# Kernel optimization log

Hardware: AMD Instinct MI355X
Metric: run time of the kernel (lower is better)

The kernel has to match this reference:

```python
import jax, jax.numpy as jnp
import numpy as np

TOP_K = 32
SCALE_FACTOR = 8.0
NEG_INF = -1e18


def setup_inputs() -> dict:
    key = jax.random.key(0)
    kq, kk, kv = jax.random.split(key, 3)
    B, H, S, D = 2, 16, 2048, 64
    q = jax.random.normal(kq, (B, H, S, D), dtype=jnp.float32)
    k = jax.random.normal(kk, (B, H, S, D), dtype=jnp.float32)
    v = jax.random.normal(kv, (B, H, S, D), dtype=jnp.float32)
    return {"q": q, "k": k, "v": v}


def reference(q, k, v):
    # scores: [B, H, Sq, Sk]
    scores = jnp.einsum("bhqd,bhkd->bhqk", q, k) / SCALE_FACTOR
    # torch code clamps top_k against key.size()[-1] == head dim D (quirk);
    # with TOP_K=32 < D=64 the clamp is inactive.
    top_k = min(TOP_K, k.shape[-1])
    topv, _ = jax.lax.top_k(scores, top_k)            # [B,H,Sq,top_k], sorted desc
    thresh = topv[..., -1:]                            # k-th largest per query row
    mask_k = scores < thresh                           # True -> masked out
    scores = jnp.where(mask_k, NEG_INF, scores)
    attn = jax.nn.softmax(scores, axis=-1)
    context = jnp.einsum("bhqk,bhkd->bhqd", attn, v)
    return context, attn, mask_k
```

## Files before the change

### kernel.cpp

```cpp
#include <hip/hip_runtime.h>
#include <math.h>

namespace {
constexpr int kS = 2048;
constexpr int kD = 64;
constexpr int kBH = 32;
constexpr int kTopK = 32;
constexpr int kPadBins = 2112;
constexpr int kCandCap = 128;
constexpr int kKeepCap = 64;
constexpr size_t kCtxElems  = (size_t)kBH * kS * kD;
constexpr size_t kAttnElems = (size_t)kBH * kS * kS;
}

typedef float f2 __attribute__((ext_vector_type(2)));

__device__ __forceinline__ unsigned sortable_bits(float x) {
  unsigned u = __float_as_uint(x);
  return u ^ ((u & 0x80000000u) ? 0xFFFFFFFFu : 0x80000000u);
}

__global__ __launch_bounds__(256) void qk_scores(const float* __restrict__ q,
                                                 const float* __restrict__ k,
                                                 float* __restrict__ scores) {
  __shared__ float QsT[32][260];
  __shared__ float KsT[32][132];
  const int bh  = blockIdx.z;
  const int q0  = blockIdx.y * 256;
  const int k0  = blockIdx.x * 128;
  const int tid = threadIdx.x;
  const float* qg = q + ((size_t)bh * kS + q0) * kD;
  const float* kg = k + ((size_t)bh * kS + k0) * kD;

  const int ty16 = (tid >> 4) * 16;
  const int tx8  = (tid & 15) * 8;
  f2 acc[16][4] = {};

  for (int half = 0; half < 2; ++half) {
    if (half) __syncthreads();
#pragma unroll
    for (int rnd = 0; rnd < 8; ++rnd) {
      int flat = rnd * 1024 + tid * 4;
      int r = flat >> 5;
      int c = flat & 31;
      float4 qv = *(const float4*)(qg + r * kD + half * 32 + c);
      QsT[c + 0][r] = qv.x;
      QsT[c + 1][r] = qv.y;
      QsT[c + 2][r] = qv.z;
      QsT[c + 3][r] = qv.w;
    }
#pragma unroll
    for (int rnd = 0; rnd < 4; ++rnd) {
      int flat = rnd * 1024 + tid * 4;
      int r = flat >> 5;
      int c = flat & 31;
      float4 kv = *(const float4*)(kg + r * kD + half * 32 + c);
      KsT[c + 0][r] = kv.x;
      KsT[c + 1][r] = kv.y;
      KsT[c + 2][r] = kv.z;
      KsT[c + 3][r] = kv.w;
    }
    __syncthreads();

#pragma unroll
    for (int kk = 0; kk < 32; ++kk) {
      float a[16];
      f2 b[4];
      *(float4*)(&a[0])  = *(const float4*)(&QsT[kk][ty16]);
      *(float4*)(&a[4])  = *(const float4*)(&QsT[kk][ty16 + 4]);
      *(float4*)(&a[8])  = *(const float4*)(&QsT[kk][ty16 + 8]);
      *(float4*)(&a[12]) = *(const float4*)(&QsT[kk][ty16 + 12]);
      float4 b0 = *(const float4*)(&KsT[kk][tx8]);
      float4 b1 = *(const float4*)(&KsT[kk][tx8 + 4]);
      b[0] = f2{b0.x, b0.y};
      b[1] = f2{b0.z, b0.w};
      b[2] = f2{b1.x, b1.y};
      b[3] = f2{b1.z, b1.w};
#pragma unroll
      for (int i = 0; i < 16; ++i) {
        const f2 as = {a[i], a[i]};
#pragma unroll
        for (int j2 = 0; j2 < 4; ++j2)
          acc[i][j2] += as * b[j2];
      }
    }
  }

#pragma unroll
  for (int i = 0; i < 16; ++i) {
    float* orow = scores + ((size_t)bh * kS + q0 + ty16 + i) * kS + k0 + tx8;
    float4 o0 = make_float4(acc[i][0].x * 0.125f, acc[i][0].y * 0.125f,
                            acc[i][1].x * 0.125f, acc[i][1].y * 0.125f);
    float4 o1 = make_float4(acc[i][2].x * 0.125f, acc[i][2].y * 0.125f,
                            acc[i][3].x * 0.125f, acc[i][3].y * 0.125f);
    *(float4*)(orow)     = o0;
    *(float4*)(orow + 4) = o1;
  }
}

__global__ __launch_bounds__(256) void topk_softmax(const float* __restrict__ v,
                                                    float* __restrict__ ctx,
                                                    float* __restrict__ attn,
                                                    float* __restrict__ mask) {
  __shared__ unsigned s_hist[4][kPadBins];
  __shared__ float    s_cand[4][kCandCap];
  __shared__ int      s_kidx[4][kKeepCap];
  __shared__ float    s_kw[4][kKeepCap];
  __shared__ unsigned s_nc[4];

  const int tid  = threadIdx.x;
  const int wid  = tid >> 6;
  const int lane = tid & 63;
  const int row  = blockIdx.x * 4 + wid;
  const int bh   = row >> 11;
  unsigned* hist = s_hist[wid];

  const float* srow = attn + (size_t)row * kS;
  float locv[32];
#pragma unroll
  for (int g = 0; g < 8; ++g)
    *(float4*)(&locv[g * 4]) = *(const float4*)(srow + g * 256 + lane * 4);

#pragma unroll
  for (int j = 0; j < 33; ++j) hist[j * 64 + lane] = 0u;
  if (lane == 0) s_nc[wid] = 0u;

  float pmax = locv[0];
#pragma unroll
  for (int j = 0; j < 32; ++j) {
    unsigned b = sortable_bits(locv[j]) >> 21;
    atomicAdd(&hist[b + (b >> 5)], 1u);
    pmax = fmaxf(pmax, locv[j]);
  }
#pragma unroll
  for (int off = 32; off >= 1; off >>= 1)
    pmax = fmaxf(pmax, __shfl_xor(pmax, off));

  asm volatile("s_waitcnt lgkmcnt(0)" ::: "memory");

  unsigned lsum = 0;
#pragma unroll
  for (int j = 0; j < 32; ++j) lsum += hist[lane * 33 + j];
  unsigned sfx = lsum;
#pragma unroll
  for (int off = 1; off < 64; off <<= 1) {
    unsigned z = __shfl_down(sfx, off);
    if (lane + off < 64) sfx += z;
  }
  const unsigned above = sfx - lsum;

  int bstar = 0, gabove = 0;
  const bool ispiv = (sfx >= (unsigned)kTopK) && (above < (unsigned)kTopK);
  if (ispiv) {
    unsigned run = above;
    for (int j = 31; j >= 0; --j) {
      unsigned h = hist[lane * 33 + j];
      if (run < (unsigned)kTopK && run + h >= (unsigned)kTopK) {
        bstar  = lane * 32 + j;
        gabove = (int)run;
      }
      run += h;
    }
  }
  const unsigned long long pm = __ballot(ispiv);
  const int psrc = __ffsll(pm) - 1;
  bstar  = __shfl(bstar, psrc);
  gabove = __shfl(gabove, psrc);

#pragma unroll
  for (int j = 0; j < 32; ++j) {
    unsigned b = sortable_bits(locv[j]) >> 21;
    if ((int)b == bstar) {
      unsigned p = atomicAdd(&s_nc[wid], 1u);
      if (p < (unsigned)kCandCap) s_cand[wid][p] = locv[j];
    }
  }
  asm volatile("s_waitcnt lgkmcnt(0)" ::: "memory");
  const int m = (int)min(s_nc[wid], (unsigned)kCandCap);

  const float x0 = (lane < m) ? s_cand[wid][lane] : 0.0f;
  const float x1 = (lane + 64 < m) ? s_cand[wid][lane + 64] : 0.0f;
  int g0 = 0, e0 = 0, g1 = 0, e1 = 0;
  for (int j = 0; j < m; ++j) {
    float y = s_cand[wid][j];
    g0 += (y > x0); e0 += (y == x0);
    g1 += (y > x1); e1 += (y == x1);
  }
  const bool win0 = (lane < m) &&
                    (gabove + g0 < kTopK) && (gabove + g0 + e0 >= kTopK);
  const bool win1 = (lane + 64 < m) &&
                    (gabove + g1 < kTopK) && (gabove + g1 + e1 >= kTopK);
  const unsigned long long wm0 = __ballot(win0);
  const unsigned long long wm1 = __ballot(win1);
  float t32;
  if (wm0 != 0ull)      t32 = __shfl(x0, __ffsll(wm0) - 1);
  else if (wm1 != 0ull) t32 = __shfl(x1, __ffsll(wm1) - 1);
  else                  t32 = pmax;

  const unsigned long long below = (1ull << lane) - 1ull;
  float w32[32];
  float psum = 0.0f;
  int nkbase = 0;
#pragma unroll
  for (int j = 0; j < 32; ++j) {
    const bool keep = (locv[j] >= t32);
    const float wv = keep ? __expf(locv[j] - pmax) : 0.0f;
    w32[j] = wv;
    psum += wv;
    const unsigned long long mk = __ballot(keep);
    if (keep) {
      const int slot = nkbase + (int)__popcll(mk & below);
      if (slot < kKeepCap) {
        s_kidx[wid][slot] = (j >> 2) * 256 + lane * 4 + (j & 3);
        s_kw[wid][slot]   = wv;
      }
    }
    nkbase += (int)__popcll(mk);
  }
  const int nk = nkbase < kKeepCap ? nkbase : kKeepCap;
#pragma unroll
  for (int off = 32; off >= 1; off >>= 1)
    psum += __shfl_xor(psum, off);
  const float invZ = 1.0f / psum;

  float* arow = attn + (size_t)row * kS;
  float* mrow = mask + (size_t)row * kS;
#pragma unroll
  for (int g = 0; g < 8; ++g) {
    float4 a = make_float4(w32[g*4+0] * invZ, w32[g*4+1] * invZ,
                           w32[g*4+2] * invZ, w32[g*4+3] * invZ);
    float4 mm = make_float4(locv[g*4+0] >= t32 ? 0.f : 1.f,
                            locv[g*4+1] >= t32 ? 0.f : 1.f,
                            locv[g*4+2] >= t32 ? 0.f : 1.f,
                            locv[g*4+3] >= t32 ? 0.f : 1.f);
    *(float4*)(arow + g * 256 + lane * 4) = a;
    *(float4*)(mrow + g * 256 + lane * 4) = mm;
  }

  asm volatile("s_waitcnt lgkmcnt(0)" ::: "memory");
  const float* vb = v + ((size_t)bh * kS) * kD + lane;
  float acc = 0.0f;
  int c = 0;
  for (; c + 8 <= nk; c += 8) {
    float w[8], vv[8];
    int   ii[8];
#pragma unroll
    for (int u = 0; u < 8; ++u) {
      w[u]  = s_kw[wid][c + u];
      ii[u] = s_kidx[wid][c + u];
    }
#pragma unroll
    for (int u = 0; u < 8; ++u)
      vv[u] = vb[(size_t)ii[u] * kD];
#pragma unroll
    for (int u = 0; u < 8; ++u)
      acc += w[u] * vv[u];
  }
  for (; c < nk; ++c)
    acc += s_kw[wid][c] * vb[(size_t)s_kidx[wid][c] * kD];
  ctx[(size_t)row * kD + lane] = acc * invZ;
}

extern "C" void kernel_launch(void* const* d_in, const int* in_sizes, int n_in,
                              void* d_out, int out_size, void* d_ws, size_t ws_size,
                              hipStream_t stream) {
  const float* q = (const float*)d_in[0];
  const float* k = (const float*)d_in[1];
  const float* v = (const float*)d_in[2];
  float* out  = (float*)d_out;
  float* ctx  = out;
  float* attn = out + kCtxElems;
  float* mask = attn + kAttnElems;

  dim3 g1(kS / 128, kS / 256, kBH);
  qk_scores<<<g1, 256, 0, stream>>>(q, k, attn);
  topk_softmax<<<dim3(kBH * kS / 4), 256, 0, stream>>>(v, ctx, attn, mask);
}
```

Measured before the change: 1.409 ms.

## Pre-transpose Q into scratch and stream it from global in QK kernel

```diff
diff --git a/kernel.cpp b/kernel.cpp
--- a/kernel.cpp
+++ b/kernel.cpp
@@ -20,81 +20,89 @@
   return u ^ ((u & 0x80000000u) ? 0xFFFFFFFFu : 0x80000000u);
 }
 
-__global__ __launch_bounds__(256) void qk_scores(const float* __restrict__ q,
-                                                 const float* __restrict__ k,
-                                                 float* __restrict__ scores) {
-  __shared__ float QsT[32][260];
-  __shared__ float KsT[32][132];
+__global__ __launch_bounds__(256) void qt_transpose(const float* __restrict__ q,
+                                                    float* __restrict__ qt) {
+  __shared__ float T[kD][130];
+  const int bh  = blockIdx.z;
+  const int r0  = blockIdx.x * 128;
+  const int tid = threadIdx.x;
+  const float* qg = q + ((size_t)bh * kS + r0) * kD;
+#pragma unroll
+  for (int rnd = 0; rnd < 8; ++rnd) {
+    int flat = rnd * 1024 + tid * 4;
+    int r = flat >> 6, c = flat & 63;
+    float4 v = *(const float4*)(qg + flat);
+    T[c + 0][r] = v.x; T[c + 1][r] = v.y;
+    T[c + 2][r] = v.z; T[c + 3][r] = v.w;
+  }
+  __syncthreads();
+  const int wid = tid >> 6, lane = tid & 63;
+#pragma unroll
+  for (int p = 0; p < 8; ++p) {
+    int d = p * 8 + wid * 2 + (lane >> 5);
+    int j = (lane & 31) * 4;
+    float4 vv = *(const float4*)(&T[d][j]);
+    *(float4*)(qt + ((size_t)(bh * kD + d)) * kS + r0 + j) = vv;
+  }
+}
+
+__global__ __launch_bounds__(256, 2) void qk_scores(const float* __restrict__ qt,
+                                                    const float* __restrict__ k,
+                                                    float* __restrict__ scores) {
+  __shared__ float KsT[kD][132];
   const int bh  = blockIdx.z;
   const int q0  = blockIdx.y * 256;
   const int k0  = blockIdx.x * 128;
   const int tid = threadIdx.x;
-  const float* qg = q + ((size_t)bh * kS + q0) * kD;
   const float* kg = k + ((size_t)bh * kS + k0) * kD;
 
+#pragma unroll
+  for (int rnd = 0; rnd < 8; ++rnd) {
+    int flat = rnd * 1024 + tid * 4;
+    int r = flat >> 6;
+    int c = flat & 63;
+    int pr = r ^ (((c >> 2) & 7) << 2);
+    float4 kv = *(const float4*)(kg + flat);
+    KsT[c + 0][pr] = kv.x; KsT[c + 1][pr] = kv.y;
+    KsT[c + 2][pr] = kv.z; KsT[c + 3][pr] = kv.w;
+  }
+  __syncthreads();
+
   const int ty16 = (tid >> 4) * 16;
-  const int tx8  = (tid & 15) * 8;
+  const int tx4  = (tid & 15) * 4;
+  const float* qtb = qt + ((size_t)bh * kD) * kS + q0 + ty16;
   f2 acc[16][4] = {};
 
-  for (int half = 0; half < 2; ++half) {
-    if (half) __syncthreads();
-#pragma unroll
-    for (int rnd = 0; rnd < 8; ++rnd) {
-      int flat = rnd * 1024 + tid * 4;
-      int r = flat >> 5;
-      int c = flat & 31;
-      float4 qv = *(const float4*)(qg + r * kD + half * 32 + c);
-      QsT[c + 0][r] = qv.x;
-      QsT[c + 1][r] = qv.y;
-      QsT[c + 2][r] = qv.z;
-      QsT[c + 3][r] = qv.w;
-    }
-#pragma unroll
-    for (int rnd = 0; rnd < 4; ++rnd) {
-      int flat = rnd * 1024 + tid * 4;
-      int r = flat >> 5;
-      int c = flat & 31;
-      float4 kv = *(const float4*)(kg + r * kD + half * 32 + c);
-      KsT[c + 0][r] = kv.x;
-      KsT[c + 1][r] = kv.y;
-      KsT[c + 2][r] = kv.z;
-      KsT[c + 3][r] = kv.w;
-    }
-    __syncthreads();
-
-#pragma unroll
-    for (int kk = 0; kk < 32; ++kk) {
-      float a[16];
-      f2 b[4];
-      *(float4*)(&a[0])  = *(const float4*)(&QsT[kk][ty16]);
-      *(float4*)(&a[4])  = *(const float4*)(&QsT[kk][ty16 + 4]);
-      *(float4*)(&a[8])  = *(const float4*)(&QsT[kk][ty16 + 8]);
-      *(float4*)(&a[12]) = *(const float4*)(&QsT[kk][ty16 + 12]);
-      float4 b0 = *(const float4*)(&KsT[kk][tx8]);
-      float4 b1 = *(const float4*)(&KsT[kk][tx8 + 4]);
-      b[0] = f2{b0.x, b0.y};
-      b[1] = f2{b0.z, b0.w};
-      b[2] = f2{b1.x, b1.y};
-      b[3] = f2{b1.z, b1.w};
-#pragma unroll
-      for (int i = 0; i < 16; ++i) {
-        const f2 as = {a[i], a[i]};
-#pragma unroll
-        for (int j2 = 0; j2 < 4; ++j2)
-          acc[i][j2] += as * b[j2];
-      }
+#pragma unroll 4
+  for (int kk = 0; kk < kD; ++kk) {
+    float a[16];
+    const float* qrow = qtb + (size_t)kk * kS;
+    *(float4*)(&a[0])  = *(const float4*)(qrow);
+    *(float4*)(&a[4])  = *(const float4*)(qrow + 4);
+    *(float4*)(&a[8])  = *(const float4*)(qrow + 8);
+    *(float4*)(&a[12]) = *(const float4*)(qrow + 12);
+    const int p = tx4 ^ (((kk >> 2) & 7) << 2);
+    float4 b0 = *(const float4*)(&KsT[kk][p]);
+    float4 b1 = *(const float4*)(&KsT[kk][64 + p]);
+    f2 b[4] = {{b0.x, b0.y}, {b0.z, b0.w}, {b1.x, b1.y}, {b1.z, b1.w}};
+#pragma unroll
+    for (int i = 0; i < 16; ++i) {
+      const f2 as = {a[i], a[i]};
+#pragma unroll
+      for (int j2 = 0; j2 < 4; ++j2)
+        acc[i][j2] += as * b[j2];
     }
   }
 
 #pragma unroll
   for (int i = 0; i < 16; ++i) {
-    float* orow = scores + ((size_t)bh * kS + q0 + ty16 + i) * kS + k0 + tx8;
+    float* orow = scores + ((size_t)bh * kS + q0 + ty16 + i) * kS + k0;
     float4 o0 = make_float4(acc[i][0].x * 0.125f, acc[i][0].y * 0.125f,
                             acc[i][1].x * 0.125f, acc[i][1].y * 0.125f);
     float4 o1 = make_float4(acc[i][2].x * 0.125f, acc[i][2].y * 0.125f,
                             acc[i][3].x * 0.125f, acc[i][3].y * 0.125f);
-    *(float4*)(orow)     = o0;
-    *(float4*)(orow + 4) = o1;
+    *(float4*)(orow + tx4)      = o0;
+    *(float4*)(orow + 64 + tx4) = o1;
   }
 }
 
@@ -272,7 +280,9 @@
   float* attn = out + kCtxElems;
   float* mask = attn + kAttnElems;
 
-  dim3 g1(kS / 128, kS / 256, kBH);
-  qk_scores<<<g1, 256, 0, stream>>>(q, k, attn);
+  float* qtscratch = mask;
+
+  qt_transpose<<<dim3(kS / 128, 1, kBH), 256, 0, stream>>>(q, qtscratch);
+  qk_scores<<<dim3(kS / 128, kS / 256, kBH), 256, 0, stream>>>(qtscratch, k, attn);
   topk_softmax<<<dim3(kBH * kS / 4), 256, 0, stream>>>(v, ctx, attn, mask);
 }
```

Result: slower. 1.459 ms (+3.5%).
